# Kernel optimization log

Hardware: AMD Instinct MI355X
Metric: run time of the kernel (lower is better)

## Reference

```python
import jax, jax.numpy as jnp
import numpy as np

VOCAB = 50257
EMBED_DIM = 128
TOP_N = 8
B, LQ, LC = 4, 128, 65536


def setup_inputs() -> dict:
    key = jax.random.key(0)
    k1, k2, k3, k4 = jax.random.split(key, 4)
    query_tokens = jax.random.randint(k1, (B, LQ), 0, VOCAB, dtype=jnp.int32)
    context_tokens = jax.random.randint(k2, (LC,), 0, VOCAB, dtype=jnp.int32)
    emb_table = jax.random.normal(k3, (VOCAB, EMBED_DIM), dtype=jnp.float32) * 0.02
    W_score = jax.random.normal(k4, (EMBED_DIM, EMBED_DIM), dtype=jnp.float32) / np.sqrt(EMBED_DIM)
    b_score = jnp.zeros((EMBED_DIM,), dtype=jnp.float32)
    return {
        "query_tokens": query_tokens,
        "context_tokens": context_tokens,
        "emb_table": emb_table,
        "W_score": W_score,
        "b_score": b_score,
    }


def reference(query_tokens, context_tokens, emb_table, W_score, b_score):
    # --- TokenEmbedder: embedding lookups ---
    q = emb_table[query_tokens]        # [B, Lq, D]
    c = emb_table[context_tokens]      # [Lc, D]

    # --- ExploratoryMechanism: euclidean distance + top_n nearest ---
    # ||q - c||^2 = ||q||^2 + ||c||^2 - 2 q.c
    sq = (jnp.sum(q * q, axis=-1)[..., None]
          + jnp.sum(c * c, axis=-1)[None, None, :]
          - 2.0 * jnp.einsum('bqd,cd->bqc', q, c))      # [B, Lq, Lc]
    dist = jnp.sqrt(jnp.maximum(sq, 0.0) + 1e-12)
    neg_top, top_n_indices = jax.lax.top_k(-dist, TOP_N)  # smallest distances
    top_n_distances = -neg_top                             # [B, Lq, n]

    # --- gather top-n context embeddings ---
    top_n_embeddings = c[top_n_indices]                    # [B, Lq, n, D]

    # --- RAGScorer: projected dot-product score penalized by distance ---
    qp = q @ W_score + b_score                             # [B, Lq, D]
    logits = (jnp.einsum('bqd,bqnd->bqn', qp, top_n_embeddings)
              / np.sqrt(EMBED_DIM)) - top_n_distances      # [B, Lq, n]
    rag_scores = jax.nn.softmax(logits, axis=-1)           # [B, Lq, n]

    # --- QueryReconstructor: score-driven reweighting of query positions ---
    importance = jnp.max(rag_scores, axis=-1)              # [B, Lq]
    weights = jax.nn.softmax(importance, axis=-1)          # [B, Lq]
    lq = query_tokens.shape[1]
    reconstructed_query = query_tokens.astype(jnp.float32) * weights * lq
    return reconstructed_query
```

## Files before the change

### kernel.cpp

```cpp
#include <hip/hip_runtime.h>
#include <math.h>

#define D      128
#define NQ     512
#define LCTX   65536
#define TOPN   8
#define NCAND  16
#define QT     128
#define CCHUNK 512
#define CSTEP  128
#define NCH    (LCTX / CCHUNK)
#define PERCHUNK 16
#define NCANDTOT (NCH * PERCHUNK)
#define NQT    (NQ / QT)
#define NROWS  (LCTX + NQ)
#define PACKB  (NROWS / 8)
#define QPREPB (NQ / 8)
#define FINF   3.0e38f

typedef __attribute__((ext_vector_type(8))) __bf16 bf16x8;
typedef __attribute__((ext_vector_type(4))) float f32x4;

static __device__ __forceinline__ unsigned pack2(float a, float b) {
  const unsigned ua = (__float_as_uint(a) + 0x8000u) >> 16;
  const unsigned ub = (__float_as_uint(b) + 0x8000u) & 0xffff0000u;
  return ua | ub;
}

__global__ __launch_bounds__(256) void prep_kernel(const int* __restrict__ ctok,
                                                   const int* __restrict__ qtok,
                                                   const float* __restrict__ emb,
                                                   const float* __restrict__ W,
                                                   const float* __restrict__ bvec,
                                                   unsigned short* __restrict__ cemb,
                                                   float* __restrict__ cn2,
                                                   float* __restrict__ qp) {
  __shared__ float sW[32 * D];
  __shared__ float sq[8][D];
  const int tid = threadIdx.x;

  if (blockIdx.x < PACKB) {
    const int g = tid >> 5, l = tid & 31;
    const int row = blockIdx.x * 8 + g;
    const int tok = (row < LCTX) ? ctok[row] : qtok[row - LCTX];
    const float4 v = *(const float4*)(emb + (size_t)tok * D + 4 * l);
    float p = v.x * v.x + v.y * v.y + v.z * v.z + v.w * v.w;
#pragma unroll
    for (int off = 16; off; off >>= 1) p += __shfl_xor(p, off, 32);
    if (l == 0 && row < LCTX) cn2[row] = p;
    const int c = l >> 1, h = l & 1;
    const int pch = c ^ (row & 7);
    uint2 pk = make_uint2(pack2(v.x, v.y), pack2(v.z, v.w));
    *(uint2*)(&cemb[(size_t)row * D + pch * 8 + h * 4]) = pk;
    return;
  }

  const int qb = (blockIdx.x - PACKB) * 8;
  {
    const int r = tid >> 5, l = tid & 31;
    const int tok = qtok[qb + r];
    *(float4*)(&sq[r][4 * l]) = *(const float4*)(emb + (size_t)tok * D + 4 * l);
  }
  const int d = tid & 127, qs = tid >> 7;
  const float bv = bvec[d];
  float acc[4] = {bv, bv, bv, bv};
  for (int ch = 0; ch < 4; ++ch) {
    __syncthreads();
#pragma unroll
    for (int j = 0; j < 4; ++j) {
      const int i4 = j * 256 + tid;
      *(float4*)(&sW[i4 * 4]) = *(const float4*)(W + (size_t)ch * 32 * D + i4 * 4);
    }
    __syncthreads();
#pragma unroll
    for (int kk = 0; kk < 32; ++kk) {
      const float wv = sW[kk * D + d];
      const int k = ch * 32 + kk;
#pragma unroll
      for (int i = 0; i < 4; ++i) acc[i] = fmaf(sq[2 * i + qs][k], wv, acc[i]);
    }
  }
#pragma unroll
  for (int i = 0; i < 4; ++i) qp[(size_t)(qb + 2 * i + qs) * D + d] = acc[i];
}

__global__ __launch_bounds__(512, 4) void dist_topk_kernel(
    const unsigned short* __restrict__ cemb, const float* __restrict__ cn2,
    float2* __restrict__ partials) {
  __shared__ __align__(16) unsigned short sCt[CSTEP * D];
  __shared__ __align__(16) float scn2[CCHUNK];

  const int tid = threadIdx.x;
  const int wid = tid >> 6, lane = tid & 63;
  const int n = lane & 15, qq = lane >> 4;
  const int chunk = blockIdx.x, qtile = blockIdx.y;
  const int qbase = qtile * QT, cbase0 = chunk * CCHUNK;

  scn2[tid] = cn2[cbase0 + tid];

  {
    const unsigned short* qrowbase = cemb + (size_t)(LCTX + qbase) * D;
#pragma unroll
    for (int j = 0; j < 4; ++j) {
      const int r0 = wid * 16 + j * 4;
      const unsigned short* gp = qrowbase + r0 * D + lane * 8;
      __builtin_amdgcn_global_load_lds(
          (const __attribute__((address_space(1))) unsigned int*)gp,
          (__attribute__((address_space(3))) unsigned int*)&sCt[r0 * D], 16, 0, 0);
    }
  }
  __syncthreads();

  bf16x8 bq[4];
  {
    const int rq = wid * 16 + n;
#pragma unroll
    for (int kk = 0; kk < 4; ++kk)
      bq[kk] = *(const bf16x8*)(&sCt[rq * D + 8 * ((4 * kk + qq) ^ (rq & 7))]);
  }

  float bs[4] = {FINF, FINF, FINF, FINF};
  int bi[4] = {0, 0, 0, 0};

  for (int st = 0; st < CCHUNK / CSTEP; ++st) {
    const int cb = cbase0 + st * CSTEP;
    __syncthreads();
    {
      const unsigned short* crowbase = cemb + (size_t)cb * D;
#pragma unroll
      for (int j = 0; j < 4; ++j) {
        const int r0 = wid * 16 + j * 4;
        const unsigned short* gp = crowbase + r0 * D + lane * 8;
        __builtin_amdgcn_global_load_lds(
            (const __attribute__((address_space(1))) unsigned int*)gp,
            (__attribute__((address_space(3))) unsigned int*)&sCt[r0 * D], 16, 0, 0);
      }
    }
    __syncthreads();

#pragma unroll
    for (int tt = 0; tt < 8; ++tt) {
      f32x4 acc = {0.f, 0.f, 0.f, 0.f};
      const int m = 16 * tt + n;
#pragma unroll
      for (int kk = 0; kk < 4; ++kk) {
        const bf16x8 af = *(const bf16x8*)(&sCt[m * D + 8 * ((4 * kk + qq) ^ (n & 7))]);
        acc = __builtin_amdgcn_mfma_f32_16x16x32_bf16(af, bq[kk], acc, 0, 0, 0);
      }
      const f32x4 cv = *(const f32x4*)(&scn2[st * CSTEP + 16 * tt + 4 * qq]);
      const int ibase = cb + 16 * tt + 4 * qq;
#pragma unroll
      for (int r = 0; r < 4; ++r) {
        const float v = fmaf(-2.f, acc[r], cv[r]);
        const int iv = ibase + r;
        const bool c0 = v < bs[0], c1 = v < bs[1], c2 = v < bs[2], c3 = v < bs[3];
        const float nb0 = fminf(bs[0], v);
        const float nb1 = __builtin_amdgcn_fmed3f(v, bs[0], bs[1]);
        const float nb2 = __builtin_amdgcn_fmed3f(v, bs[1], bs[2]);
        const float nb3 = __builtin_amdgcn_fmed3f(v, bs[2], bs[3]);
        const int ni0 = c0 ? iv : bi[0];
        const int ni1 = c1 ? (c0 ? bi[0] : iv) : bi[1];
        const int ni2 = c2 ? (c1 ? bi[1] : iv) : bi[2];
        const int ni3 = c3 ? (c2 ? bi[2] : iv) : bi[3];
        bs[0] = nb0; bs[1] = nb1; bs[2] = nb2; bs[3] = nb3;
        bi[0] = ni0; bi[1] = ni1; bi[2] = ni2; bi[3] = ni3;
      }
    }
  }

  const int q = qbase + wid * 16 + n;
  float2* dst = partials + (size_t)q * NCANDTOT + chunk * PERCHUNK + qq * 4;
#pragma unroll
  for (int t = 0; t < 4; ++t)
    dst[t] = make_float2(bs[t], __int_as_float(bi[t]));
}

__global__ __launch_bounds__(256) void select_kernel(
    const float2* __restrict__ partials, const int* __restrict__ qtok,
    const int* __restrict__ ctok, const float* __restrict__ emb,
    const float* __restrict__ qp, float* __restrict__ importance) {
  __shared__ float2 swt[64];
  __shared__ double sd2[NCAND], sdp[NCAND];
  __shared__ int sid[NCAND];
  const int tid = threadIdx.x;
  const int w = tid >> 6, lane = tid & 63;
  const int q = blockIdx.x;

  float v[8]; int vi[8];
  const float4* pq4 = (const float4*)(partials + (size_t)q * NCANDTOT);
#pragma unroll
  for (int j = 0; j < 4; ++j) {
    const float4 cd = pq4[256 * j + tid];
    v[2 * j] = cd.x;     vi[2 * j] = __float_as_int(cd.y);
    v[2 * j + 1] = cd.z; vi[2 * j + 1] = __float_as_int(cd.w);
  }
  unsigned consumed = 0;
#pragma unroll
  for (int t = 0; t < NCAND; ++t) {
    float lmin = FINF; int li = 0x7fffffff; int ls = 0;
#pragma unroll
    for (int j = 0; j < 8; ++j) {
      const bool take = !((consumed >> j) & 1u) && (v[j] < lmin);
      lmin = take ? v[j] : lmin;
      li = take ? vi[j] : li;
      ls = take ? j : ls;
    }
    float m = lmin; int pidx = li; int pwho = (lane << 3) | ls;
#pragma unroll
    for (int off = 32; off; off >>= 1) {
      const float om = __shfl_xor(m, off, 64);
      const int oi = __shfl_xor(pidx, off, 64);
      const int ow = __shfl_xor(pwho, off, 64);
      const bool better = (om < m) || (om == m && oi < pidx);
      m = better ? om : m; pidx = better ? oi : pidx; pwho = better ? ow : pwho;
    }
    if ((pwho >> 3) == lane) consumed |= 1u << (pwho & 7);
    if (lane == t) swt[w * 16 + t] = make_float2(m, __int_as_float(pidx));
  }
  __syncthreads();

  if (w == 0) {
    const float2 cd = swt[lane];
    const float mv = cd.x; const int mi = __float_as_int(cd.y);
    bool cons = false;
#pragma unroll
    for (int t = 0; t < NCAND; ++t) {
      float m = cons ? FINF : mv;
      int pidx = cons ? 0x7fffffff : mi;
      int pwho = lane;
#pragma unroll
      for (int off = 32; off; off >>= 1) {
        const float om = __shfl_xor(m, off, 64);
        const int oi = __shfl_xor(pidx, off, 64);
        const int ow = __shfl_xor(pwho, off, 64);
        const bool better = (om < m) || (om == m && oi < pidx);
        m = better ? om : m; pidx = better ? oi : pidx; pwho = better ? ow : pwho;
      }
      if (pwho == lane) cons = true;
      if (lane == t) sid[t] = pidx;
    }
  }
  __syncthreads();

  const int c = tid >> 4, sub = tid & 15;
  const int idx = sid[c];
  const int tc = ctok[idx];
  const int tq = qtok[q];
  const float* crow = emb + (size_t)tc * D + sub * 8;
  const float* qrow = emb + (size_t)tq * D + sub * 8;
  const float* prow = qp + (size_t)q * D + sub * 8;
  double dd = 0.0, pp = 0.0;
#pragma unroll
  for (int kk = 0; kk < 2; ++kk) {
    const float4 cv = *(const float4*)(crow + 4 * kk);
    const float4 qv = *(const float4*)(qrow + 4 * kk);
    const float4 pv = *(const float4*)(prow + 4 * kk);
    const double dx = (double)qv.x - (double)cv.x, dy = (double)qv.y - (double)cv.y;
    const double dz = (double)qv.z - (double)cv.z, dw = (double)qv.w - (double)cv.w;
    dd += dx * dx + dy * dy + dz * dz + dw * dw;
    pp += (double)pv.x * (double)cv.x + (double)pv.y * (double)cv.y +
          (double)pv.z * (double)cv.z + (double)pv.w * (double)cv.w;
  }
#pragma unroll
  for (int off = 1; off <= 8; off <<= 1) {
    dd += __shfl_xor(dd, off, 64);
    pp += __shfl_xor(pp, off, 64);
  }
  if (sub == 0) { sd2[c] = dd; sdp[c] = pp; }
  __syncthreads();

  if (w == 0 && lane < NCAND) {
    const double d2 = sd2[lane];
    const double dp = sdp[lane];
    const int cid = sid[lane];
    int rank = 0;
#pragma unroll
    for (int off = 1; off < NCAND; ++off) {
      const double od = __shfl_xor(d2, off, 64);
      const int oc = __shfl_xor(cid, off, 64);
      rank += (od < d2 || (od == d2 && oc < cid)) ? 1 : 0;
    }
    const bool sel = (rank < TOPN);
    const double lg = sel
        ? dp * 0.08838834764831843 - sqrt(d2 + 1e-12)
        : -1.0e300;
    double mx = lg;
#pragma unroll
    for (int off = 1; off <= 8; off <<= 1) mx = fmax(mx, __shfl_xor(mx, off, 64));
    const double e = sel ? exp(lg - mx) : 0.0;
    double s = e;
#pragma unroll
    for (int off = 1; off <= 8; off <<= 1) s += __shfl_xor(s, off, 64);
    if (lane == 0) importance[q] = (float)(1.0 / s);
  }
}

__global__ __launch_bounds__(128) void out_kernel(const float* __restrict__ importance,
                                                  const int* __restrict__ qtok,
                                                  float* __restrict__ out) {
  const int b = blockIdx.x, i = threadIdx.x;
  __shared__ double sred[2];
  const double v = (double)importance[b * 128 + i];
  double m = v;
#pragma unroll
  for (int off = 32; off; off >>= 1) m = fmax(m, __shfl_xor(m, off, 64));
  if ((i & 63) == 0) sred[i >> 6] = m;
  __syncthreads();
  const double M = fmax(sred[0], sred[1]);
  const double e = exp(v - M);
  double s = e;
#pragma unroll
  for (int off = 32; off; off >>= 1) s += __shfl_xor(s, off, 64);
  __syncthreads();
  if ((i & 63) == 0) sred[i >> 6] = s;
  __syncthreads();
  const double S = sred[0] + sred[1];
  out[b * 128 + i] = (float)((double)qtok[b * 128 + i] * (e / S) * 128.0);
}

extern "C" void kernel_launch(void* const* d_in, const int* in_sizes, int n_in,
                              void* d_out, int out_size, void* d_ws, size_t ws_size,
                              hipStream_t stream) {
  const int* qtok = (const int*)d_in[0];
  const int* ctok = (const int*)d_in[1];
  const float* emb = (const float*)d_in[2];
  const float* W = (const float*)d_in[3];
  const float* bvec = (const float*)d_in[4];
  float* out = (float*)d_out;

  char* ws = (char*)d_ws;
  float* cn2 = (float*)ws;
  float* qp = cn2 + LCTX;
  float* imp = qp + (size_t)NQ * D;
  unsigned short* cemb = (unsigned short*)(imp + NQ);
  float2* partials = (float2*)(cemb + (size_t)NROWS * D);

  prep_kernel<<<PACKB + QPREPB, 256, 0, stream>>>(ctok, qtok, emb, W, bvec,
                                                  cemb, cn2, qp);
  dist_topk_kernel<<<dim3(NCH, NQT), 512, 0, stream>>>(cemb, cn2, partials);
  select_kernel<<<NQ, 256, 0, stream>>>(partials, qtok, ctok, emb, qp, imp);
  out_kernel<<<4, 128, 0, stream>>>(imp, qtok, out);
}
```

Measured before the change: 142.5 us.

## Merge per-chunk candidates across lanes to keep only top four per chunk

```diff
diff --git a/kernel.cpp b/kernel.cpp
--- a/kernel.cpp
+++ b/kernel.cpp
@@ -10,7 +10,7 @@
 #define CCHUNK 512
 #define CSTEP  128
 #define NCH    (LCTX / CCHUNK)
-#define PERCHUNK 16
+#define PERCHUNK 4
 #define NCANDTOT (NCH * PERCHUNK)
 #define NQT    (NQ / QT)
 #define NROWS  (LCTX + NQ)
@@ -168,11 +168,27 @@
     }
   }
 
+  int rank[4] = {0, 1, 2, 3};
+#pragma unroll
+  for (int off = 16; off <= 48; off += 16) {
+    float os[4]; int oi[4];
+#pragma unroll
+    for (int t = 0; t < 4; ++t) {
+      os[t] = __shfl_xor(bs[t], off, 64);
+      oi[t] = __shfl_xor(bi[t], off, 64);
+    }
+#pragma unroll
+    for (int j = 0; j < 4; ++j)
+#pragma unroll
+      for (int t = 0; t < 4; ++t)
+        rank[j] += (os[t] < bs[j] || (os[t] == bs[j] && oi[t] < bi[j])) ? 1 : 0;
+  }
   const int q = qbase + wid * 16 + n;
-  float2* dst = partials + (size_t)q * NCANDTOT + chunk * PERCHUNK + qq * 4;
-#pragma unroll
-  for (int t = 0; t < 4; ++t)
-    dst[t] = make_float2(bs[t], __int_as_float(bi[t]));
+#pragma unroll
+  for (int j = 0; j < 4; ++j)
+    if (rank[j] < PERCHUNK)
+      partials[(size_t)q * NCANDTOT + chunk * PERCHUNK + rank[j]] =
+          make_float2(bs[j], __int_as_float(bi[j]));
 }
 
 __global__ __launch_bounds__(256) void select_kernel(
@@ -186,26 +202,22 @@
   const int w = tid >> 6, lane = tid & 63;
   const int q = blockIdx.x;
 
-  float v[8]; int vi[8];
-  const float4* pq4 = (const float4*)(partials + (size_t)q * NCANDTOT);
-#pragma unroll
-  for (int j = 0; j < 4; ++j) {
-    const float4 cd = pq4[256 * j + tid];
-    v[2 * j] = cd.x;     vi[2 * j] = __float_as_int(cd.y);
-    v[2 * j + 1] = cd.z; vi[2 * j + 1] = __float_as_int(cd.w);
+  float v[2]; int vi[2];
+  {
+    const float4 cd = ((const float4*)(partials + (size_t)q * NCANDTOT))[tid];
+    v[0] = cd.x; vi[0] = __float_as_int(cd.y);
+    v[1] = cd.z; vi[1] = __float_as_int(cd.w);
   }
   unsigned consumed = 0;
 #pragma unroll
   for (int t = 0; t < NCAND; ++t) {
-    float lmin = FINF; int li = 0x7fffffff; int ls = 0;
-#pragma unroll
-    for (int j = 0; j < 8; ++j) {
-      const bool take = !((consumed >> j) & 1u) && (v[j] < lmin);
-      lmin = take ? v[j] : lmin;
-      li = take ? vi[j] : li;
-      ls = take ? j : ls;
-    }
-    float m = lmin; int pidx = li; int pwho = (lane << 3) | ls;
+    float lmin; int li; int ls;
+    const bool t0 = !(consumed & 1u), t1 = !(consumed & 2u);
+    const bool pick1 = t1 && (!t0 || v[1] < v[0]);
+    lmin = pick1 ? v[1] : (t0 ? v[0] : FINF);
+    li = pick1 ? vi[1] : (t0 ? vi[0] : 0x7fffffff);
+    ls = pick1 ? 1 : 0;
+    float m = lmin; int pidx = li; int pwho = (lane << 1) | ls;
 #pragma unroll
     for (int off = 32; off; off >>= 1) {
       const float om = __shfl_xor(m, off, 64);
@@ -214,7 +226,7 @@
       const bool better = (om < m) || (om == m && oi < pidx);
       m = better ? om : m; pidx = better ? oi : pidx; pwho = better ? ow : pwho;
     }
-    if ((pwho >> 3) == lane) consumed |= 1u << (pwho & 7);
+    if ((pwho >> 1) == lane) consumed |= 1u << (pwho & 1);
     if (lane == t) swt[w * 16 + t] = make_float2(m, __int_as_float(pidx));
   }
   __syncthreads();
```

New measurement: 142.8 us. No clear change (+0.2%).
